# Optimization experiments

Hardware: AMD Instinct MI355X
Metric: run time of the kernel (lower is better)

Reference implementation:

```python
import jax, jax.numpy as jnp
import numpy as np

POSITIVE_MULT = 3.0  # init kwarg positive_mult
MIN_K = 10


def _ohem_single(pred, tgt):
    """OHEM MSE for one flattened sample. pred, tgt: [N]."""
    N = pred.shape[0]
    loss = (pred - tgt) ** 2  # elementwise MSE (reduction='none')
    pos = tgt > 0
    num_pos = jnp.sum(pos.astype(jnp.int32))
    # k = num_pos * positive_mult, clamped so k + num_pos <= N  =>  k = min(3p, N-p)
    k = jnp.minimum((num_pos.astype(jnp.float32) * POSITIVE_MULT).astype(jnp.int32),
                    N - num_pos)
    full_mean = jnp.mean(loss)
    # positive mean (safe denom; branch unused when num_pos small => k < 10)
    pos_mean = jnp.sum(jnp.where(pos, loss, 0.0)) / jnp.maximum(num_pos, 1).astype(loss.dtype)
    # top-k over negative losses: mask positives to -inf, sort descending,
    # take first k via index mask (k is traced, so no dynamic shapes)
    neg_loss = jnp.where(pos, -jnp.inf, loss)
    sorted_desc = -jnp.sort(-neg_loss)
    idx = jnp.arange(N)
    topk_mean = jnp.sum(jnp.where(idx < k, sorted_desc, 0.0)) / jnp.maximum(k, 1).astype(loss.dtype)
    ohem = pos_mean + topk_mean
    return jnp.where(k < MIN_K, full_mean, ohem)


def reference(x, char_target, aff_target):
    B, _, H, W = x.shape
    pred_r = x[:, 0].reshape(B, -1)  # region scores
    pred_a = x[:, 1].reshape(B, -1)  # affinity scores
    # bilinear resize, half-pixel centers == torch align_corners=False
    ct = jax.image.resize(char_target, (B, 1, H, W), method='bilinear').reshape(B, -1)
    at = jax.image.resize(aff_target, (B, 1, H, W), method='bilinear').reshape(B, -1)
    char_loss = jax.vmap(_ohem_single)(pred_r, ct)  # [B]
    aff_loss = jax.vmap(_ohem_single)(pred_a, at)   # [B]
    return jnp.mean(char_loss + aff_loss)


def setup_inputs() -> dict:
    key = jax.random.key(0)
    k1, k2, k3 = jax.random.split(key, 3)
    x = jax.random.normal(k1, (32, 2, 640, 640), dtype=jnp.float32)
    char_target = jax.random.normal(k2, (32, 1, 320, 320), dtype=jnp.float32)
    aff_target = jax.random.normal(k3, (32, 1, 320, 320), dtype=jnp.float32)
    return {"x": x, "char_target": char_target, "aff_target": aff_target}
```

## Files before the change

kernel.cpp:

```cpp
#include <hip/hip_runtime.h>

#define NS 64
#define HH 640
#define WW 640
#define NPIX (HH * WW)
#define TH 320
#define TW 320
#define MINK 10
#define BPS 40
#define TPB 320
#define ITERS 4

__device__ __forceinline__ float resize_scalar(const float* __restrict__ tgt, int y, int xc) {
    float sy = fmaxf(0.5f * (float)y - 0.25f, 0.0f);
    int y0 = (int)sy;
    float fy = sy - (float)y0;
    int y1 = min(y0 + 1, TH - 1);
    float sx = fmaxf(0.5f * (float)xc - 0.25f, 0.0f);
    int x0 = (int)sx;
    float fx = sx - (float)x0;
    int x1 = min(x0 + 1, TW - 1);
    const float* r0 = tgt + y0 * TW;
    const float* r1 = tgt + y1 * TW;
    float top = (1.0f - fx) * r0[x0] + fx * r0[x1];
    float bot = (1.0f - fx) * r1[x0] + fx * r1[x1];
    return (1.0f - fy) * top + fy * bot;
}

__global__ __launch_bounds__(TPB) void k_reduce(const float* __restrict__ x,
                                                const float* __restrict__ ct,
                                                const float* __restrict__ at,
                                                float* __restrict__ partA,
                                                float* __restrict__ partP,
                                                int* __restrict__ partC) {
    int bid = blockIdx.x;
    int s = bid / BPS, blk = bid % BPS;
    int b = s >> 1, c = s & 1;
    const float* pred = x + (size_t)s * NPIX;
    const float* tgt = (c == 0 ? ct : at) + (size_t)b * (TH * TW);

    int tid = threadIdx.x;
    int u = tid % 80;
    int rr = tid / 80;
    int rbase = blk * 16;

    float fy = (rr & 1) ? 0.25f : 0.75f;
    float gy = 1.0f - fy;
    int xq = 4 * u;
    int xl = max(xq - 1, 0);
    int xr = min(xq + 4, TW - 1);

    float sA = 0.0f, sP = 0.0f;
    int cP = 0;

#pragma unroll
    for (int i = 0; i < ITERS; ++i) {
        int y = rbase + rr + 4 * i;
        int y0raw = (y >> 1) + (y & 1) - 1;
        int y0 = max(y0raw, 0);
        int y1 = min(y0raw + 1, TH - 1);
        const float* r0 = tgt + y0 * TW;
        const float* r1 = tgt + y1 * TW;

        float4 a4 = *reinterpret_cast<const float4*>(r0 + xq);
        float La = r0[xl], Ra = r0[xr];
        float4 b4 = *reinterpret_cast<const float4*>(r1 + xq);
        float Lb = r1[xl], Rb = r1[xr];

        float mL = gy * La + fy * Lb;
        float m0 = gy * a4.x + fy * b4.x;
        float m1 = gy * a4.y + fy * b4.y;
        float m2 = gy * a4.z + fy * b4.z;
        float m3 = gy * a4.w + fy * b4.w;
        float mR = gy * Ra + fy * Rb;

        float tv[8];
        tv[0] = 0.25f * mL + 0.75f * m0;
        tv[1] = 0.75f * m0 + 0.25f * m1;
        tv[2] = 0.25f * m0 + 0.75f * m1;
        tv[3] = 0.75f * m1 + 0.25f * m2;
        tv[4] = 0.25f * m1 + 0.75f * m2;
        tv[5] = 0.75f * m2 + 0.25f * m3;
        tv[6] = 0.25f * m2 + 0.75f * m3;
        tv[7] = 0.75f * m3 + 0.25f * mR;

        const float* pr = pred + y * WW + 8 * u;
        float4 p0 = *reinterpret_cast<const float4*>(pr);
        float4 p1 = *reinterpret_cast<const float4*>(pr + 4);
        float pv[8] = {p0.x, p0.y, p0.z, p0.w, p1.x, p1.y, p1.z, p1.w};

#pragma unroll
        for (int j = 0; j < 8; ++j) {
            float d = pv[j] - tv[j];
            float l = d * d;
            sA += l;
            bool pos = tv[j] > 0.0f;
            sP += pos ? l : 0.0f;
            cP += pos ? 1 : 0;
        }
    }

    for (int off = 32; off > 0; off >>= 1) {
        sA += __shfl_down(sA, off);
        sP += __shfl_down(sP, off);
        cP += __shfl_down(cP, off);
    }
    __shared__ float shA[5], shP[5];
    __shared__ int shC[5];
    int w = tid >> 6;
    if ((tid & 63) == 0) { shA[w] = sA; shP[w] = sP; shC[w] = cP; }
    __syncthreads();
    if (tid == 0) {
        float a = 0.0f, p = 0.0f;
        int ci = 0;
        for (int q = 0; q < 5; ++q) { a += shA[q]; p += shP[q]; ci += shC[q]; }
        partA[s * BPS + blk] = a;
        partP[s * BPS + blk] = p;
        partC[s * BPS + blk] = ci;
    }
}

__global__ __launch_bounds__(TPB) void k_tail(const float* __restrict__ x,
                                              const float* __restrict__ ct,
                                              const float* __restrict__ at,
                                              const float* __restrict__ partA,
                                              const float* __restrict__ partP,
                                              const int* __restrict__ partC,
                                              float* __restrict__ out) {
    int tid = threadIdx.x;
    __shared__ float lossSh[NS];
    __shared__ int flagSh[NS], pSh[NS];

    if (tid < NS) {
        float a = 0.0f, pp = 0.0f;
        int p = 0;
        const float4* pa4 = reinterpret_cast<const float4*>(partA + tid * BPS);
        const float4* pp4 = reinterpret_cast<const float4*>(partP + tid * BPS);
        const int4*   pc4 = reinterpret_cast<const int4*>(partC + tid * BPS);
#pragma unroll
        for (int q = 0; q < BPS / 4; ++q) {
            float4 va = pa4[q]; a += va.x + va.y + va.z + va.w;
            float4 vp = pp4[q]; pp += vp.x + vp.y + vp.z + vp.w;
            int4 vc = pc4[q]; p += vc.x + vc.y + vc.z + vc.w;
        }
        int k = min((int)((float)p * 3.0f), NPIX - p);
        pSh[tid] = p;
        flagSh[tid] = (k >= MINK && k < NPIX - p) ? 1 : 0;
        float lossv;
        if (k < MINK) {
            lossv = a / (float)NPIX;
        } else {
            float nn = a - pp;
            float ts = (k >= NPIX - p) ? nn : 0.0f;
            lossv = pp / (float)max(p, 1) + ts / (float)max(k, 1);
        }
        lossSh[tid] = lossv;
    }
    __syncthreads();

    __shared__ unsigned int hcnt[2048];
    __shared__ float hsum[2048];
    __shared__ unsigned int selBin, remSh;
    __shared__ float sumTopSh;
    for (int s2 = 0; s2 < NS; ++s2) {
        if (!flagSh[s2]) continue;
        int p2 = pSh[s2];
        int k2 = min((int)((float)p2 * 3.0f), NPIX - p2);
        const float* pred2 = x + (size_t)s2 * NPIX;
        const float* tgt2 = ((s2 & 1) == 0 ? ct : at) + (size_t)(s2 >> 1) * (TH * TW);
        if (tid == 0) { remSh = (unsigned int)k2; sumTopSh = 0.0f; }
        const int shiftv[3] = {21, 10, 0};
        const unsigned int maskv[3] = {0x7FFu, 0x7FFu, 0x3FFu};
        unsigned int prefix = 0;
        for (int pass = 0; pass < 3; ++pass) {
            for (int i = tid; i < 2048; i += TPB) { hcnt[i] = 0u; hsum[i] = 0.0f; }
            __syncthreads();
            for (int e = tid; e < NPIX; e += TPB) {
                int yy = e / WW, xx = e % WW;
                float tv = resize_scalar(tgt2, yy, xx);
                if (tv > 0.0f) continue;
                float d = pred2[e] - tv;
                float l = d * d;
                unsigned int bits = __float_as_uint(l);
                bool match;
                if (pass == 0) match = true;
                else if (pass == 1) match = ((bits >> 21) == prefix);
                else match = ((bits >> 10) == prefix);
                if (match) {
                    unsigned int bin = (bits >> shiftv[pass]) & maskv[pass];
                    atomicAdd(&hcnt[bin], 1u);
                    atomicAdd(&hsum[bin], l);
                }
            }
            __syncthreads();
            if (tid == 0) {
                unsigned int remS = remSh;
                int nb = (int)maskv[pass] + 1;
                unsigned int cum = 0; float sAb = 0.0f; unsigned int bsel = 0;
                for (int bin = nb - 1; bin >= 0; --bin) {
                    unsigned int cc = hcnt[bin];
                    if (cum + cc >= remS) { bsel = (unsigned int)bin; break; }
                    cum += cc; sAb += hsum[bin];
                }
                selBin = bsel;
                remSh = remS - cum;
                sumTopSh += sAb;
            }
            __syncthreads();
            if (pass == 0) prefix = selBin;
            else if (pass == 1) prefix = (prefix << 11) | selBin;
            __syncthreads();
        }
        if (tid == 0) {
            unsigned int bits = (prefix << 10) | selBin;
            float topk = sumTopSh + (float)remSh * __uint_as_float(bits);
            lossSh[s2] += topk / (float)max(k2, 1);
        }
        __syncthreads();
    }

    if (tid < NS) {
        float lossv = lossSh[tid];
        for (int off = 32; off > 0; off >>= 1) lossv += __shfl_down(lossv, off);
        if (tid == 0) out[0] = lossv / 32.0f;
    }
}

extern "C" void kernel_launch(void* const* d_in, const int* in_sizes, int n_in,
                              void* d_out, int out_size, void* d_ws, size_t ws_size,
                              hipStream_t stream) {
    const float* x  = (const float*)d_in[0];
    const float* ct = (const float*)d_in[1];
    const float* at = (const float*)d_in[2];
    float* out = (float*)d_out;

    float* partA = (float*)d_ws;
    float* partP = partA + NS * BPS;
    int*   partC = (int*)(partP + NS * BPS);

    k_reduce<<<dim3(NS * BPS), dim3(TPB), 0, stream>>>(x, ct, at, partA, partP, partC);
    k_tail<<<dim3(1), dim3(TPB), 0, stream>>>(x, ct, at, partA, partP, partC, out);
}
```

Baseline: 32.67 us.

## Stage vertically interpolated target rows in swizzled shared memory

Each block now loads the ten source target rows it needs once, with one coalesced column per thread, and performs the vertical bilinear pass into a padded, swizzled LDS tile of 16 output rows. The horizontal pass then reads from LDS instead of issuing repeated overlapping global loads of the same target rows for each output row. This removes redundant global and L2 traffic and the per-iteration vertical arithmetic, at the cost of about 21 KB of LDS per block and a __syncthreads barrier before the main loop.

```diff
diff --git a/kernel.cpp b/kernel.cpp
--- a/kernel.cpp
+++ b/kernel.cpp
@@ -9,7 +9,9 @@
 #define MINK 10
 #define BPS 40
 #define TPB 320
-#define ITERS 4
+#define LSTR 330
+
+__device__ __forceinline__ int swz(int q) { return q + (q >> 5); }
 
 __device__ __forceinline__ float resize_scalar(const float* __restrict__ tgt, int y, int xc) {
     float sy = fmaxf(0.5f * (float)y - 0.25f, 0.0f);
@@ -40,39 +42,47 @@
     const float* tgt = (c == 0 ? ct : at) + (size_t)b * (TH * TW);
 
     int tid = threadIdx.x;
-    int u = tid % 80;
-    int rr = tid / 80;
+    __shared__ float sm[16 * LSTR];
+
+    {
+        int cc = tid;
+        int h = blk * 8;
+        float rowv[10];
+#pragma unroll
+        for (int r = 0; r < 10; ++r) {
+            int ri = min(max(h - 1 + r, 0), TH - 1);
+            rowv[r] = tgt[ri * TW + cc];
+        }
+        int sc = swz(cc);
+#pragma unroll
+        for (int j = 0; j < 16; ++j) {
+            int l0 = (j >> 1) + (j & 1);
+            float fy = (j & 1) ? 0.25f : 0.75f;
+            sm[j * LSTR + sc] = (1.0f - fy) * rowv[l0] + fy * rowv[l0 + 1];
+        }
+    }
+    __syncthreads();
+
+    int u = tid % 80, rr = tid / 80;
     int rbase = blk * 16;
-
-    float fy = (rr & 1) ? 0.25f : 0.75f;
-    float gy = 1.0f - fy;
     int xq = 4 * u;
-    int xl = max(xq - 1, 0);
-    int xr = min(xq + 4, TW - 1);
+    int sL = swz(max(xq - 1, 0));
+    int s0 = swz(xq);
+    int sR = swz(min(xq + 4, TW - 1));
 
     float sA = 0.0f, sP = 0.0f;
     int cP = 0;
 
 #pragma unroll
-    for (int i = 0; i < ITERS; ++i) {
-        int y = rbase + rr + 4 * i;
-        int y0raw = (y >> 1) + (y & 1) - 1;
-        int y0 = max(y0raw, 0);
-        int y1 = min(y0raw + 1, TH - 1);
-        const float* r0 = tgt + y0 * TW;
-        const float* r1 = tgt + y1 * TW;
-
-        float4 a4 = *reinterpret_cast<const float4*>(r0 + xq);
-        float La = r0[xl], Ra = r0[xr];
-        float4 b4 = *reinterpret_cast<const float4*>(r1 + xq);
-        float Lb = r1[xl], Rb = r1[xr];
-
-        float mL = gy * La + fy * Lb;
-        float m0 = gy * a4.x + fy * b4.x;
-        float m1 = gy * a4.y + fy * b4.y;
-        float m2 = gy * a4.z + fy * b4.z;
-        float m3 = gy * a4.w + fy * b4.w;
-        float mR = gy * Ra + fy * Rb;
+    for (int i = 0; i < 4; ++i) {
+        int j = rr + 4 * i;
+        const float* mr = sm + j * LSTR;
+        float mL = mr[sL];
+        float m0 = mr[s0];
+        float m1 = mr[s0 + 1];
+        float m2 = mr[s0 + 2];
+        float m3 = mr[s0 + 3];
+        float mR = mr[sR];
 
         float tv[8];
         tv[0] = 0.25f * mL + 0.75f * m0;
@@ -84,17 +94,17 @@
         tv[6] = 0.25f * m2 + 0.75f * m3;
         tv[7] = 0.75f * m3 + 0.25f * mR;
 
-        const float* pr = pred + y * WW + 8 * u;
+        const float* pr = pred + (rbase + j) * WW + 8 * u;
         float4 p0 = *reinterpret_cast<const float4*>(pr);
         float4 p1 = *reinterpret_cast<const float4*>(pr + 4);
         float pv[8] = {p0.x, p0.y, p0.z, p0.w, p1.x, p1.y, p1.z, p1.w};
 
 #pragma unroll
-        for (int j = 0; j < 8; ++j) {
-            float d = pv[j] - tv[j];
+        for (int t = 0; t < 8; ++t) {
+            float d = pv[t] - tv[t];
             float l = d * d;
             sA += l;
-            bool pos = tv[j] > 0.0f;
+            bool pos = tv[t] > 0.0f;
             sP += pos ? l : 0.0f;
             cP += pos ? 1 : 0;
         }
```

After: 32.04 us. About the same (-1.9%).
